# Kernel tuning notes

Hardware: AMD Instinct MI355X
Metric: run time of the kernel (lower is better)

The kernel has to match this reference:

```python
import jax, jax.numpy as jnp
import numpy as np
from jax import lax

N = 4096      # nodes
D = 256       # in_channels
H = 128       # hidden_size (cell output = 2*H = 256)
BLOCK = 128   # row-block size for the masked-max scan
THR = 0.99    # adjacency threshold on uniform A -> avg degree ~41
EPS = 1e-12


def _block_max(m, scores):
    # m: [BLOCK, N] bool, scores: [N, H] -> [BLOCK, H]
    v = jnp.where(m[:, :, None], scores[None, :, :], -jnp.inf)
    return v.max(axis=1)

_block_max = jax.checkpoint(_block_max)


def masked_max(mask, scores):
    # maxpool over neighbors, blocked over destination nodes to avoid an [N,N,H] temp
    n = mask.shape[0]
    mblk = mask.reshape(n // BLOCK, BLOCK, n)
    def body(_, m):
        return None, _block_max(m, scores)
    _, out = lax.scan(body, None, mblk)
    out = out.reshape(n, scores.shape[-1])
    # nodes with no neighbors -> 0
    return jnp.where(jnp.isneginf(out), jnp.zeros_like(out), out)


def setup_inputs() -> dict:
    key = jax.random.key(0)
    ks = jax.random.split(key, 16)
    def w(k, shape):
        fan = shape[0]
        return (jax.random.normal(k, shape, jnp.float32) / np.sqrt(fan)).astype(jnp.float32)
    D1 = 2 * H  # layer-1 input dim (= 256)
    return dict(
        x=jax.random.normal(ks[0], (N, D), jnp.float32),
        A=jax.random.uniform(ks[1], (N, N), dtype=jnp.float32),
        # layer 0 cell params
        Wp0=w(ks[2], (D, H)), bp0=jnp.zeros((H,), jnp.float32),
        Ws0=w(ks[3], (D, H)), bs0=jnp.zeros((H,), jnp.float32),
        Wn0=w(ks[4], (H, H)), bn0=jnp.zeros((H,), jnp.float32),
        # layer 1 cell params
        Wp1=w(ks[5], (D1, H)), bp1=jnp.zeros((H,), jnp.float32),
        Ws1=w(ks[6], (D1, H)), bs1=jnp.zeros((H,), jnp.float32),
        Wn1=w(ks[7], (H, H)), bn1=jnp.zeros((H,), jnp.float32),
    )


def _cell(x, mask, Wp, bp, Ws, bs, Wn, bn):
    # GraphSAGE maxpool cell: concat(self transform, neighbor maxpool transform)
    scores = jax.nn.relu(x @ Wp + bp)                 # [N, H]
    pooled = masked_max(mask, scores)                 # [N, H]
    return jnp.concatenate([x @ Ws + bs, pooled @ Wn + bn], axis=-1)  # [N, 2H]


def reference(x, A, Wp0, bp0, Ws0, bs0, Wn0, bn0, Wp1, bp1, Ws1, bs1, Wn1, bn1):
    mask = A > THR  # [N, N] bool adjacency
    for (Wp, bp, Ws, bs, Wn, bn) in ((Wp0, bp0, Ws0, bs0, Wn0, bn0),
                                     (Wp1, bp1, Ws1, bs1, Wn1, bn1)):
        x = _cell(x, mask, Wp, bp, Ws, bs, Wn, bn)
        x = jax.nn.relu(x)
        nrm = jnp.linalg.norm(x, axis=-1, keepdims=True)
        x = x / jnp.maximum(nrm, EPS)
    return x
```

## Files before the change

### kernel.cpp

```cpp
#include <hip/hip_runtime.h>

#define NN 4096
#define CAP 256
#define THRV 0.99f

typedef __attribute__((ext_vector_type(8))) short short8v;
typedef __attribute__((ext_vector_type(4))) float f32x4;

__device__ inline unsigned short f2bf(float f) {
  unsigned u = __builtin_bit_cast(unsigned, f);
  u = (u + 0x7fffu + ((u >> 16) & 1u)) >> 16;
  return (unsigned short)u;
}
__device__ inline unsigned pkmax(unsigned a, unsigned b) {
  unsigned r;
  asm("v_pk_max_u16 %0, %1, %2" : "=v"(r) : "v"(a), "v"(b));
  return r;
}
__device__ inline uint4 max4(uint4 a, uint4 b) {
  return make_uint4(pkmax(a.x, b.x), pkmax(a.y, b.y), pkmax(a.z, b.z), pkmax(a.w, b.w));
}


#define GEMM_BLKS 128
#define PREP_BLKS 96
#define SCAN_BLKS 512

__global__ __launch_bounds__(256) void kA(
    const float* __restrict__ x, const float* __restrict__ A,
    const float* __restrict__ Wp0, const float* __restrict__ bp0,
    const float* __restrict__ Ws0, const float* __restrict__ bs0,
    const float* __restrict__ Wn0, const float* __restrict__ Wp1,
    const float* __restrict__ Ws1, const float* __restrict__ Wn1,
    int* __restrict__ cnt, unsigned short* __restrict__ nbr,
    unsigned short* __restrict__ scores0, float* __restrict__ S0,
    unsigned short* __restrict__ tWn0, unsigned short* __restrict__ tWp1,
    unsigned short* __restrict__ tWs1, unsigned short* __restrict__ tWn1) {
  const int bid = blockIdx.x;
  if (bid < GEMM_BLKS) {
    const int wv = threadIdx.x >> 6, lane = threadIdx.x & 63;
    const int unit = bid * 4 + wv;
    const int set = unit >> 8;
    const int rb = unit & 255;
    const float* W = set ? Ws0 : Wp0;
    const float* bias = set ? bs0 : bp0;
    const int g = lane >> 4, r15 = lane & 15;
    const int row = rb * 16 + r15;
    f32x4 acc[8] = {};
    for (int kt = 0; kt < 256; kt += 32) {
      const float* xp = x + (size_t)row * 256 + kt + 4 * g;
      float4 lo = *(const float4*)xp;
      float4 hi = *(const float4*)(xp + 16);
      short8v a;
      a[0] = (short)f2bf(lo.x); a[1] = (short)f2bf(lo.y);
      a[2] = (short)f2bf(lo.z); a[3] = (short)f2bf(lo.w);
      a[4] = (short)f2bf(hi.x); a[5] = (short)f2bf(hi.y);
      a[6] = (short)f2bf(hi.z); a[7] = (short)f2bf(hi.w);
#pragma unroll
      for (int nf = 0; nf < 8; ++nf) {
        const float* wp = W + (size_t)(kt + 4 * g) * 128 + nf * 16 + r15;
        short8v b;
#pragma unroll
        for (int j = 0; j < 4; ++j) b[j] = (short)f2bf(wp[(size_t)j * 128]);
#pragma unroll
        for (int j = 0; j < 4; ++j) b[4 + j] = (short)f2bf(wp[(size_t)(16 + j) * 128]);
        acc[nf] = __builtin_amdgcn_mfma_f32_16x16x32_bf16(a, b, acc[nf], 0, 0, 0);
      }
    }
#pragma unroll
    for (int nf = 0; nf < 8; ++nf) {
      int col = nf * 16 + r15;
      float bv = bias[col];
#pragma unroll
      for (int r = 0; r < 4; ++r) {
        int orow = rb * 16 + 4 * g + r;
        float t = acc[nf][r] + bv;
        if (set == 0) scores0[(size_t)orow * 128 + col] = f2bf(fmaxf(t, 0.f));
        else          S0[(size_t)orow * 128 + col] = t;
      }
    }
    return;
  }
  if (bid < GEMM_BLKS + PREP_BLKS) {
    int id = bid - GEMM_BLKS;
    const float* src; unsigned short* dst; int base;
    if (id < 16)      { src = Wn0; dst = tWn0; base = id; }
    else if (id < 48) { src = Wp1; dst = tWp1; base = id - 16; }
    else if (id < 80) { src = Ws1; dst = tWs1; base = id - 48; }
    else              { src = Wn1; dst = tWn1; base = id - 80; }
    int e0 = base * 1024 + threadIdx.x * 4;
    float4 v = *(const float4*)(src + e0);
    int k = e0 >> 7, n = e0 & 127;
    float vv[4] = {v.x, v.y, v.z, v.w};
    int elem = (k & 3) + 4 * ((k >> 4) & 1);
    int gg = (k >> 2) & 3;
    int fragkt = (k >> 5) * 8;
#pragma unroll
    for (int i = 0; i < 4; ++i) {
      int nn = n + i;
      int idx = ((fragkt + (nn >> 4)) << 9) + ((gg * 16 + (nn & 15)) << 3) + elem;
      dst[idx] = f2bf(vv[i]);
    }
    return;
  }
  {
    __shared__ int scnt[8];
    __shared__ unsigned short snb[8][CAP];
    const int t = threadIdx.x;
    const int lane = t & 63;
    const int r0 = (bid - GEMM_BLKS - PREP_BLKS) * 8;
    if (t < 8) scnt[t] = 0;
    __syncthreads();
    const float4* base = (const float4*)(A + (size_t)r0 * NN) + 4 * t;
    float4 c0 = base[0], c1 = base[1], c2 = base[2], c3 = base[3];
    for (int r = 0; r < 8; ++r) {
      float4 n0 = c0, n1 = c1, n2 = c2, n3 = c3;
      if (r < 7) {
        const float4* nb = base + (size_t)(r + 1) * (NN / 4);
        n0 = nb[0]; n1 = nb[1]; n2 = nb[2]; n3 = nb[3];
      }
      unsigned m = 0;
      m |= (c0.x > THRV) ? 0x1u : 0u;    m |= (c0.y > THRV) ? 0x2u : 0u;
      m |= (c0.z > THRV) ? 0x4u : 0u;    m |= (c0.w > THRV) ? 0x8u : 0u;
      m |= (c1.x > THRV) ? 0x10u : 0u;   m |= (c1.y > THRV) ? 0x20u : 0u;
      m |= (c1.z > THRV) ? 0x40u : 0u;   m |= (c1.w > THRV) ? 0x80u : 0u;
      m |= (c2.x > THRV) ? 0x100u : 0u;  m |= (c2.y > THRV) ? 0x200u : 0u;
      m |= (c2.z > THRV) ? 0x400u : 0u;  m |= (c2.w > THRV) ? 0x800u : 0u;
      m |= (c3.x > THRV) ? 0x1000u : 0u; m |= (c3.y > THRV) ? 0x2000u : 0u;
      m |= (c3.z > THRV) ? 0x4000u : 0u; m |= (c3.w > THRV) ? 0x8000u : 0u;
      int cntT = __popc(m);
      int inc = cntT;
#pragma unroll
      for (int off = 1; off < 64; off <<= 1) {
        int o = __shfl_up(inc, off, 64);
        if (lane >= off) inc += o;
      }
      int excl = inc - cntT;
      int wtot = __shfl(inc, 63, 64);
      int wbase = 0;
      if (lane == 0) wbase = atomicAdd(&scnt[r], wtot);
      wbase = __shfl(wbase, 0, 64);
      int pos = wbase + excl;
      while (m) {
        int i = __ffs(m) - 1;
        m &= m - 1;
        if (pos < CAP) snb[r][pos] = (unsigned short)(16 * t + i);
        ++pos;
      }
      c0 = n0; c1 = n1; c2 = n2; c3 = n3;
    }
    __syncthreads();
    if (t < 8) cnt[r0 + t] = min(scnt[t], CAP);
    {
      ushort4* dst = (ushort4*)(nbr + (size_t)r0 * CAP);
      const ushort4* s = (const ushort4*)snb;
      dst[t] = s[t];
      dst[t + 256] = s[t + 256];
    }
  }
}

template<int LAYER>
__global__ __launch_bounds__(512) void fusedL(
    const int* __restrict__ cnt, const unsigned short* __restrict__ nbr,
    const unsigned short* __restrict__ scores_in, const float* __restrict__ S_in,
    const unsigned short* __restrict__ tWn, const float* __restrict__ bn,
    const unsigned short* __restrict__ tWp, const float* __restrict__ bp,
    const unsigned short* __restrict__ tWs, const float* __restrict__ bs,
    unsigned short* __restrict__ scores_out, float* __restrict__ S_out,
    float* __restrict__ out) {
  __shared__ int scnt[16];
  __shared__ unsigned short snb[16][CAP];
  __shared__ unsigned short pool2[16][2][136];
  __shared__ unsigned short pooled[16][136];
  __shared__ unsigned short xb[16][264];
  __shared__ float ssqs[16];
  __shared__ float ssqw[4][16];

  const int tid = threadIdx.x;
  const int wv = tid >> 6, lane = tid & 63, g = lane >> 4, r15 = lane & 15;
  const int r0 = blockIdx.x * 16;

  if (tid < 16) scnt[tid] = cnt[r0 + tid];
  {
    const ushort4* src = (const ushort4*)(nbr + (size_t)r0 * CAP);
    ushort4* dst = (ushort4*)snb;
    dst[tid] = src[tid];
    dst[tid + 512] = src[tid + 512];
  }
  __syncthreads();

  {
    const int r = tid >> 5, sub = tid & 31;
    const int h = sub >> 4, c8 = (sub & 15) * 8;
    const int c = scnt[r];
    uint4 m0 = make_uint4(0, 0, 0, 0), m1 = m0, m2 = m0, m3 = m0;
    int k = h;
    for (; k + 6 < c; k += 8) {
      int j0 = snb[r][k], j1 = snb[r][k + 2], j2 = snb[r][k + 4], j3 = snb[r][k + 6];
      uint4 a0 = *(const uint4*)(scores_in + (size_t)j0 * 128 + c8);
      uint4 a1 = *(const uint4*)(scores_in + (size_t)j1 * 128 + c8);
      uint4 a2 = *(const uint4*)(scores_in + (size_t)j2 * 128 + c8);
      uint4 a3 = *(const uint4*)(scores_in + (size_t)j3 * 128 + c8);
      m0 = max4(m0, a0); m1 = max4(m1, a1); m2 = max4(m2, a2); m3 = max4(m3, a3);
    }
    for (; k < c; k += 2)
      m0 = max4(m0, *(const uint4*)(scores_in + (size_t)snb[r][k] * 128 + c8));
    *(uint4*)&pool2[r][h][c8] = max4(max4(m0, m1), max4(m2, m3));
  }
  __syncthreads();
  if (tid < 256) {
    const int r = tid >> 4, c8 = (tid & 15) * 8;
    uint4 a = *(const uint4*)&pool2[r][0][c8];
    uint4 b = *(const uint4*)&pool2[r][1][c8];
    *(uint4*)&pooled[r][c8] = max4(a, b);
  }
  __syncthreads();

  float sv[8];
  f32x4 pacc[2] = {};
  const int srow = tid >> 4, sc8 = (tid & 15) * 8;
  if (tid < 256) {
    const float* sp = S_in + (size_t)(r0 + srow) * 128 + sc8;
    float4 sa = *(const float4*)sp;
    float4 sb = *(const float4*)(sp + 4);
    sv[0] = fmaxf(sa.x, 0.f); sv[1] = fmaxf(sa.y, 0.f);
    sv[2] = fmaxf(sa.z, 0.f); sv[3] = fmaxf(sa.w, 0.f);
    sv[4] = fmaxf(sb.x, 0.f); sv[5] = fmaxf(sb.y, 0.f);
    sv[6] = fmaxf(sb.z, 0.f); sv[7] = fmaxf(sb.w, 0.f);
    float ps = 0.f;
#pragma unroll
    for (int i = 0; i < 8; ++i) ps += sv[i] * sv[i];
#pragma unroll
    for (int off = 1; off < 16; off <<= 1) ps += __shfl_xor(ps, off, 16);
    if ((tid & 15) == 0) ssqs[srow] = ps;
  } else {
    const int wv2 = wv - 4;
#pragma unroll
    for (int kt = 0; kt < 128; kt += 32) {
      ushort4 alo = *(const ushort4*)&pooled[r15][kt + 4 * g];
      ushort4 ahi = *(const ushort4*)&pooled[r15][kt + 16 + 4 * g];
      short8v a;
      a[0] = alo.x; a[1] = alo.y; a[2] = alo.z; a[3] = alo.w;
      a[4] = ahi.x; a[5] = ahi.y; a[6] = ahi.z; a[7] = ahi.w;
#pragma unroll
      for (int f = 0; f < 2; ++f) {
        uint4 bw = *((const uint4*)(tWn + (size_t)((kt >> 5) * 8 + 2 * wv2 + f) * 512) + lane);
        pacc[f] = __builtin_amdgcn_mfma_f32_16x16x32_bf16(a, __builtin_bit_cast(short8v, bw), pacc[f], 0, 0, 0);
      }
    }
#pragma unroll
    for (int f = 0; f < 2; ++f) {
      float bv = bn[(2 * wv2 + f) * 16 + r15];
#pragma unroll
      for (int rr = 0; rr < 4; ++rr) pacc[f][rr] = fmaxf(pacc[f][rr] + bv, 0.f);
    }
#pragma unroll
    for (int rr = 0; rr < 4; ++rr) {
      float ps = pacc[0][rr] * pacc[0][rr] + pacc[1][rr] * pacc[1][rr];
#pragma unroll
      for (int off = 1; off < 16; off <<= 1) ps += __shfl_xor(ps, off, 16);
      if (r15 == 0) ssqw[wv2][4 * g + rr] = ps;
    }
  }
  __syncthreads();

  if (LAYER == 0) {
    if (tid < 256) {
      float tot = ssqs[srow] + ssqw[0][srow] + ssqw[1][srow] + ssqw[2][srow] + ssqw[3][srow];
      float sc = 1.f / fmaxf(sqrtf(tot), 1e-12f);
      unsigned short hh[8];
#pragma unroll
      for (int i = 0; i < 8; ++i) hh[i] = f2bf(sv[i] * sc);
      uint4 wvv;
      wvv.x = (unsigned)hh[0] | ((unsigned)hh[1] << 16);
      wvv.y = (unsigned)hh[2] | ((unsigned)hh[3] << 16);
      wvv.z = (unsigned)hh[4] | ((unsigned)hh[5] << 16);
      wvv.w = (unsigned)hh[6] | ((unsigned)hh[7] << 16);
      *(uint4*)&xb[srow][sc8] = wvv;
    } else {
      const int wv2 = wv - 4;
#pragma unroll
      for (int rr = 0; rr < 4; ++rr) {
        int row = 4 * g + rr;
        float tot = ssqs[row] + ssqw[0][row] + ssqw[1][row] + ssqw[2][row] + ssqw[3][row];
        float sc = 1.f / fmaxf(sqrtf(tot), 1e-12f);
#pragma unroll
        for (int f = 0; f < 2; ++f)
          xb[row][128 + (2 * wv2 + f) * 16 + r15] = f2bf(pacc[f][rr] * sc);
      }
    }
    __syncthreads();
    const int s = wv >> 2;
    const unsigned short* Wt = s ? tWs : tWp;
    const float* bb = s ? bs : bp;
    const int nf0 = (wv & 3) * 2;
    f32x4 dacc[2] = {};
#pragma unroll
    for (int kt = 0; kt < 256; kt += 32) {
      ushort4 alo = *(const ushort4*)&xb[r15][kt + 4 * g];
      ushort4 ahi = *(const ushort4*)&xb[r15][kt + 16 + 4 * g];
      short8v a;
      a[0] = alo.x; a[1] = alo.y; a[2] = alo.z; a[3] = alo.w;
      a[4] = ahi.x; a[5] = ahi.y; a[6] = ahi.z; a[7] = ahi.w;
#pragma unroll
      for (int f = 0; f < 2; ++f) {
        uint4 bw = *((const uint4*)(Wt + (size_t)((kt >> 5) * 8 + nf0 + f) * 512) + lane);
        dacc[f] = __builtin_amdgcn_mfma_f32_16x16x32_bf16(a, __builtin_bit_cast(short8v, bw), dacc[f], 0, 0, 0);
      }
    }
#pragma unroll
    for (int f = 0; f < 2; ++f) {
      int col = (nf0 + f) * 16 + r15;
      float bv = bb[col];
#pragma unroll
      for (int rr = 0; rr < 4; ++rr) {
        int grow = r0 + 4 * g + rr;
        float t = dacc[f][rr] + bv;
        if (s == 0) scores_out[(size_t)grow * 128 + col] = f2bf(fmaxf(t, 0.f));
        else        S_out[(size_t)grow * 128 + col] = t;
      }
    }
  } else {
    if (tid < 256) {
      float tot = ssqs[srow] + ssqw[0][srow] + ssqw[1][srow] + ssqw[2][srow] + ssqw[3][srow];
      float sc = 1.f / fmaxf(sqrtf(tot), 1e-12f);
      float* op = out + (size_t)(r0 + srow) * 256 + sc8;
      *(float4*)op = make_float4(sv[0] * sc, sv[1] * sc, sv[2] * sc, sv[3] * sc);
      *(float4*)(op + 4) = make_float4(sv[4] * sc, sv[5] * sc, sv[6] * sc, sv[7] * sc);
    } else {
      const int wv2 = wv - 4;
#pragma unroll
      for (int rr = 0; rr < 4; ++rr) {
        int row = 4 * g + rr;
        float tot = ssqs[row] + ssqw[0][row] + ssqw[1][row] + ssqw[2][row] + ssqw[3][row];
        float sc = 1.f / fmaxf(sqrtf(tot), 1e-12f);
#pragma unroll
        for (int f = 0; f < 2; ++f)
          out[(size_t)(r0 + row) * 256 + 128 + (2 * wv2 + f) * 16 + r15] = pacc[f][rr] * sc;
      }
    }
  }
}

extern "C" void kernel_launch(void* const* d_in, const int* in_sizes, int n_in,
                              void* d_out, int out_size, void* d_ws, size_t ws_size,
                              hipStream_t stream) {
  (void)in_sizes; (void)n_in; (void)out_size; (void)ws_size;
  const float* x   = (const float*)d_in[0];
  const float* A   = (const float*)d_in[1];
  const float* Wp0 = (const float*)d_in[2];
  const float* bp0 = (const float*)d_in[3];
  const float* Ws0 = (const float*)d_in[4];
  const float* bs0 = (const float*)d_in[5];
  const float* Wn0 = (const float*)d_in[6];
  const float* bn0 = (const float*)d_in[7];
  const float* Wp1 = (const float*)d_in[8];
  const float* bp1 = (const float*)d_in[9];
  const float* Ws1 = (const float*)d_in[10];
  const float* bs1 = (const float*)d_in[11];
  const float* Wn1 = (const float*)d_in[12];
  const float* bn1 = (const float*)d_in[13];

  char* ws = (char*)d_ws;
  auto alloc = [&](size_t bytes) { char* p = ws; ws += (bytes + 255) & ~(size_t)255; return p; };
  int* cnt             = (int*)alloc((size_t)NN * 4);
  unsigned short* nbr  = (unsigned short*)alloc((size_t)NN * CAP * 2);
  unsigned short* tWn0 = (unsigned short*)alloc(128 * 128 * 2);
  unsigned short* tWp1 = (unsigned short*)alloc(256 * 128 * 2);
  unsigned short* tWs1 = (unsigned short*)alloc(256 * 128 * 2);
  unsigned short* tWn1 = (unsigned short*)alloc(128 * 128 * 2);
  unsigned short* scores0 = (unsigned short*)alloc((size_t)NN * 128 * 2);
  unsigned short* scores1 = (unsigned short*)alloc((size_t)NN * 128 * 2);
  float* S0            = (float*)alloc((size_t)NN * 128 * 4);
  float* S1            = (float*)alloc((size_t)NN * 128 * 4);

  kA<<<GEMM_BLKS + PREP_BLKS + SCAN_BLKS, 256, 0, stream>>>(
      x, A, Wp0, bp0, Ws0, bs0, Wn0, Wp1, Ws1, Wn1,
      cnt, nbr, scores0, S0, tWn0, tWp1, tWs1, tWn1);
  fusedL<0><<<NN / 16, 512, 0, stream>>>(cnt, nbr, scores0, S0,
                                         tWn0, bn0, tWp1, bp1, tWs1, bs1,
                                         scores1, S1, nullptr);
  fusedL<1><<<NN / 16, 512, 0, stream>>>(cnt, nbr, scores1, S1,
                                         tWn1, bn1, nullptr, nullptr, nullptr, nullptr,
                                         nullptr, nullptr, (float*)d_out);
}
```

Baseline: 51.60 us.

## Stage bf16 weight fragments in LDS for layer-0 GEMM and widen scan blocks

```diff
diff --git a/kernel.cpp b/kernel.cpp
--- a/kernel.cpp
+++ b/kernel.cpp
@@ -24,7 +24,7 @@
 
 #define GEMM_BLKS 128
 #define PREP_BLKS 96
-#define SCAN_BLKS 512
+#define SCAN_BLKS 256
 
 __global__ __launch_bounds__(256) void kA(
     const float* __restrict__ x, const float* __restrict__ A,
@@ -36,19 +36,41 @@
     unsigned short* __restrict__ scores0, float* __restrict__ S0,
     unsigned short* __restrict__ tWn0, unsigned short* __restrict__ tWp1,
     unsigned short* __restrict__ tWs1, unsigned short* __restrict__ tWn1) {
+  __shared__ union SM {
+    unsigned short w[32768];
+    struct { int scnt[16]; unsigned short snb[16][CAP]; } scan;
+  } sm;
   const int bid = blockIdx.x;
+  const int tid = threadIdx.x;
+
   if (bid < GEMM_BLKS) {
-    const int wv = threadIdx.x >> 6, lane = threadIdx.x & 63;
-    const int unit = bid * 4 + wv;
-    const int set = unit >> 8;
-    const int rb = unit & 255;
+    const int set = bid >> 6;
     const float* W = set ? Ws0 : Wp0;
     const float* bias = set ? bs0 : bp0;
+#pragma unroll
+    for (int it = 0; it < 32; ++it) {
+      int e0 = it * 1024 + tid * 4;
+      float4 v = *(const float4*)(W + e0);
+      int k = e0 >> 7, n = e0 & 127;
+      int elem = (k & 3) + 4 * ((k >> 4) & 1);
+      int gg = (k >> 2) & 3;
+      int kt8 = (k >> 5) * 8;
+      float vv[4] = {v.x, v.y, v.z, v.w};
+#pragma unroll
+      for (int i = 0; i < 4; ++i) {
+        int nn = n + i;
+        sm.w[((kt8 + (nn >> 4)) << 9) + ((gg * 16 + (nn & 15)) << 3) + elem] = f2bf(vv[i]);
+      }
+    }
+    __syncthreads();
+    const int wv = tid >> 6, lane = tid & 63;
     const int g = lane >> 4, r15 = lane & 15;
-    const int row = rb * 16 + r15;
+    const int rb16 = (bid & 63) * 64 + wv * 16;
+    const int row = rb16 + r15;
     f32x4 acc[8] = {};
-    for (int kt = 0; kt < 256; kt += 32) {
-      const float* xp = x + (size_t)row * 256 + kt + 4 * g;
+#pragma unroll
+    for (int ktIdx = 0; ktIdx < 8; ++ktIdx) {
+      const float* xp = x + (size_t)row * 256 + ktIdx * 32 + 4 * g;
       float4 lo = *(const float4*)xp;
       float4 hi = *(const float4*)(xp + 16);
       short8v a;
@@ -58,13 +80,8 @@
       a[6] = (short)f2bf(hi.z); a[7] = (short)f2bf(hi.w);
 #pragma unroll
       for (int nf = 0; nf < 8; ++nf) {
-        const float* wp = W + (size_t)(kt + 4 * g) * 128 + nf * 16 + r15;
-        short8v b;
-#pragma unroll
-        for (int j = 0; j < 4; ++j) b[j] = (short)f2bf(wp[(size_t)j * 128]);
-#pragma unroll
-        for (int j = 0; j < 4; ++j) b[4 + j] = (short)f2bf(wp[(size_t)(16 + j) * 128]);
-        acc[nf] = __builtin_amdgcn_mfma_f32_16x16x32_bf16(a, b, acc[nf], 0, 0, 0);
+        uint4 bw = *(const uint4*)(sm.w + ((ktIdx * 8 + nf) << 9) + lane * 8);
+        acc[nf] = __builtin_amdgcn_mfma_f32_16x16x32_bf16(a, __builtin_bit_cast(short8v, bw), acc[nf], 0, 0, 0);
       }
     }
 #pragma unroll
@@ -73,7 +90,7 @@
       float bv = bias[col];
 #pragma unroll
       for (int r = 0; r < 4; ++r) {
-        int orow = rb * 16 + 4 * g + r;
+        int orow = rb16 + 4 * g + r;
         float t = acc[nf][r] + bv;
         if (set == 0) scores0[(size_t)orow * 128 + col] = f2bf(fmaxf(t, 0.f));
         else          S0[(size_t)orow * 128 + col] = t;
@@ -88,7 +105,7 @@
     else if (id < 48) { src = Wp1; dst = tWp1; base = id - 16; }
     else if (id < 80) { src = Ws1; dst = tWs1; base = id - 48; }
     else              { src = Wn1; dst = tWn1; base = id - 80; }
-    int e0 = base * 1024 + threadIdx.x * 4;
+    int e0 = base * 1024 + tid * 4;
     float4 v = *(const float4*)(src + e0);
     int k = e0 >> 7, n = e0 & 127;
     float vv[4] = {v.x, v.y, v.z, v.w};
@@ -104,18 +121,16 @@
     return;
   }
   {
-    __shared__ int scnt[8];
-    __shared__ unsigned short snb[8][CAP];
-    const int t = threadIdx.x;
+    const int t = tid;
     const int lane = t & 63;
-    const int r0 = (bid - GEMM_BLKS - PREP_BLKS) * 8;
-    if (t < 8) scnt[t] = 0;
+    const int r0 = (bid - GEMM_BLKS - PREP_BLKS) * 16;
+    if (t < 16) sm.scan.scnt[t] = 0;
     __syncthreads();
     const float4* base = (const float4*)(A + (size_t)r0 * NN) + 4 * t;
     float4 c0 = base[0], c1 = base[1], c2 = base[2], c3 = base[3];
-    for (int r = 0; r < 8; ++r) {
+    for (int r = 0; r < 16; ++r) {
       float4 n0 = c0, n1 = c1, n2 = c2, n3 = c3;
-      if (r < 7) {
+      if (r < 15) {
         const float4* nb = base + (size_t)(r + 1) * (NN / 4);
         n0 = nb[0]; n1 = nb[1]; n2 = nb[2]; n3 = nb[3];
       }
@@ -138,24 +153,24 @@
       int excl = inc - cntT;
       int wtot = __shfl(inc, 63, 64);
       int wbase = 0;
-      if (lane == 0) wbase = atomicAdd(&scnt[r], wtot);
+      if (lane == 0) wbase = atomicAdd(&sm.scan.scnt[r], wtot);
       wbase = __shfl(wbase, 0, 64);
       int pos = wbase + excl;
       while (m) {
         int i = __ffs(m) - 1;
         m &= m - 1;
-        if (pos < CAP) snb[r][pos] = (unsigned short)(16 * t + i);
+        if (pos < CAP) sm.scan.snb[r][pos] = (unsigned short)(16 * t + i);
         ++pos;
       }
       c0 = n0; c1 = n1; c2 = n2; c3 = n3;
     }
     __syncthreads();
-    if (t < 8) cnt[r0 + t] = min(scnt[t], CAP);
+    if (t < 16) cnt[r0 + t] = min(sm.scan.scnt[t], CAP);
     {
       ushort4* dst = (ushort4*)(nbr + (size_t)r0 * CAP);
-      const ushort4* s = (const ushort4*)snb;
-      dst[t] = s[t];
-      dst[t + 256] = s[t + 256];
+      const ushort4* s = (const ushort4*)sm.scan.snb;
+#pragma unroll
+      for (int i = 0; i < 4; ++i) dst[t + 256 * i] = s[t + 256 * i];
     }
   }
 }
```

Measured after the change: 44.38 us. 14.0% less time.
